# Optimization experiments

Hardware: AMD Instinct MI355X
Metric: run time of the kernel (lower is better)

Reference implementation:

```python
import jax, jax.numpy as jnp
import numpy as np

N_NODES = 100000
N_EDGES = 3200000
D_IN = 512
D_HID = 16
N_CLS = 7


def setup_inputs() -> dict:
    key = jax.random.key(0)
    k1, k2, k3, k4, k5, k6 = jax.random.split(key, 6)
    x = jax.random.normal(k1, (N_NODES, D_IN), dtype=jnp.float32)
    edge_index = jax.random.randint(k2, (2, N_EDGES), 0, N_NODES, dtype=jnp.int64)
    # Glorot-ish init for the two GCNConv layers (normalize=False)
    W1 = jax.random.normal(k3, (D_IN, D_HID), dtype=jnp.float32) / np.sqrt(D_IN)
    b1 = jnp.zeros((D_HID,), dtype=jnp.float32)
    W2 = jax.random.normal(k4, (D_HID, N_CLS), dtype=jnp.float32) / np.sqrt(D_HID)
    b2 = jnp.zeros((N_CLS,), dtype=jnp.float32)
    return {"x": x, "edge_index": edge_index, "W1": W1, "b1": b1, "W2": W2, "b2": b2}


def gcn_conv(h, src, dst, W, b, n_nodes):
    # GCNConv with normalize=False: transform, then scatter-add x_j into dst.
    h = h @ W                                   # [N, d_out]
    msg = jnp.take(h, src, axis=0)              # [E, d_out] gather from source nodes
    agg = jax.ops.segment_sum(msg, dst, num_segments=n_nodes)  # [N, d_out]
    return agg + b


def reference(x, edge_index, W1, b1, W2, b2):
    src = edge_index[0]
    dst = edge_index[1]
    h = gcn_conv(x, src, dst, W1, b1, N_NODES)
    h = jax.nn.relu(h)
    # F.dropout(training=False) in eval mode is identity; omitted (stochastic).
    out = gcn_conv(h, src, dst, W2, b2, N_NODES)
    return out
```

## Files before the change

### kernel.cpp

```cpp
#include <hip/hip_runtime.h>

#define N_NODES 100000
#define N_EDGES 3200000
#define D_IN    512
#define D_HID   16
#define N_CLS   7

__global__ __launch_bounds__(256) void zero_f4(float4* __restrict__ p, int n4) {
    int i = blockIdx.x * 256 + threadIdx.x;
    if (i < n4) p[i] = make_float4(0.f, 0.f, 0.f, 0.f);
}

__global__ __launch_bounds__(256) void gemm1(const float* __restrict__ x,
                                             const float* __restrict__ W1,
                                             float* __restrict__ h1) {
    __shared__ float4 w4s[D_IN * 4];
    const float4* W1f4 = (const float4*)W1;
    int t = threadIdx.x;
#pragma unroll
    for (int i = 0; i < 8; ++i) w4s[i * 256 + t] = W1f4[i * 256 + t];
    __syncthreads();

    int jq  = t & 3;
    int r   = t >> 2;
    int row = blockIdx.x * 64 + r;
    if (row >= N_NODES) return;

    const float4* xr = (const float4*)(x + (size_t)row * D_IN);
    float4 acc = make_float4(0.f, 0.f, 0.f, 0.f);

#pragma unroll 4
    for (int k4 = 0; k4 < D_IN / 4; ++k4) {
        float4 xv = xr[k4];
        float4 w0 = w4s[(k4 * 4 + 0) * 4 + jq];
        float4 w1 = w4s[(k4 * 4 + 1) * 4 + jq];
        float4 w2 = w4s[(k4 * 4 + 2) * 4 + jq];
        float4 w3 = w4s[(k4 * 4 + 3) * 4 + jq];
        acc.x = fmaf(xv.x, w0.x, acc.x); acc.y = fmaf(xv.x, w0.y, acc.y);
        acc.z = fmaf(xv.x, w0.z, acc.z); acc.w = fmaf(xv.x, w0.w, acc.w);
        acc.x = fmaf(xv.y, w1.x, acc.x); acc.y = fmaf(xv.y, w1.y, acc.y);
        acc.z = fmaf(xv.y, w1.z, acc.z); acc.w = fmaf(xv.y, w1.w, acc.w);
        acc.x = fmaf(xv.z, w2.x, acc.x); acc.y = fmaf(xv.z, w2.y, acc.y);
        acc.z = fmaf(xv.z, w2.z, acc.z); acc.w = fmaf(xv.z, w2.w, acc.w);
        acc.x = fmaf(xv.w, w3.x, acc.x); acc.y = fmaf(xv.w, w3.y, acc.y);
        acc.z = fmaf(xv.w, w3.z, acc.z); acc.w = fmaf(xv.w, w3.w, acc.w);
    }
    ((float4*)(h1 + (size_t)row * D_HID))[jq] = acc;
}

__global__ __launch_bounds__(256) void scatter1(const int* __restrict__ src,
                                                const int* __restrict__ dst,
                                                const float* __restrict__ h1,
                                                float* __restrict__ agg) {
    int tid = blockIdx.x * 256 + threadIdx.x;
    int e = tid >> 4;
    int j = tid & 15;
    if (e >= N_EDGES) return;
    int s = src[e];
    int d = dst[e];
    atomicAdd(&agg[(size_t)d * D_HID + j], h1[(size_t)s * D_HID + j]);
}

__global__ __launch_bounds__(256) void layer2(const float* __restrict__ agg,
                                              const float* __restrict__ b1,
                                              const float* __restrict__ W2,
                                              float* __restrict__ h2) {
    __shared__ float w2s[D_HID * N_CLS];
    __shared__ float b1s[D_HID];
    int t = threadIdx.x;
    if (t < D_HID * N_CLS) w2s[t] = W2[t];
    if (t < D_HID) b1s[t] = b1[t];
    __syncthreads();

    int n = blockIdx.x * 256 + t;
    if (n >= N_NODES) return;

    const float4* a4 = (const float4*)(agg + (size_t)n * D_HID);
    float rel[D_HID];
#pragma unroll
    for (int q = 0; q < 4; ++q) {
        float4 v = a4[q];
        rel[4 * q + 0] = fmaxf(v.x + b1s[4 * q + 0], 0.f);
        rel[4 * q + 1] = fmaxf(v.y + b1s[4 * q + 1], 0.f);
        rel[4 * q + 2] = fmaxf(v.z + b1s[4 * q + 2], 0.f);
        rel[4 * q + 3] = fmaxf(v.w + b1s[4 * q + 3], 0.f);
    }
    float o[N_CLS];
#pragma unroll
    for (int c = 0; c < N_CLS; ++c) o[c] = 0.f;
#pragma unroll
    for (int j = 0; j < D_HID; ++j) {
#pragma unroll
        for (int c = 0; c < N_CLS; ++c)
            o[c] = fmaf(rel[j], w2s[j * N_CLS + c], o[c]);
    }
    float* hp = h2 + (size_t)n * N_CLS;
#pragma unroll
    for (int c = 0; c < N_CLS; ++c) hp[c] = o[c];
}

__global__ __launch_bounds__(256) void out_init(const float* __restrict__ b2,
                                                float* __restrict__ out) {
    int i = blockIdx.x * 256 + threadIdx.x;
    if (i >= N_NODES * N_CLS) return;
    int c = i - (i / N_CLS) * N_CLS;
    out[i] = b2[c];
}

__global__ __launch_bounds__(256) void scatter2(const int* __restrict__ src,
                                                const int* __restrict__ dst,
                                                const float* __restrict__ h2,
                                                float* __restrict__ out) {
    int tid = blockIdx.x * 256 + threadIdx.x;
    if (tid >= N_EDGES * N_CLS) return;
    int e = tid / N_CLS;
    int c = tid - e * N_CLS;
    int s = src[e];
    int d = dst[e];
    atomicAdd(&out[(size_t)d * N_CLS + c], h2[(size_t)s * N_CLS + c]);
}

extern "C" void kernel_launch(void* const* d_in, const int* in_sizes, int n_in,
                              void* d_out, int out_size, void* d_ws, size_t ws_size,
                              hipStream_t stream) {
    const float* x  = (const float*)d_in[0];
    const int*   ei = (const int*)d_in[1];
    const float* W1 = (const float*)d_in[2];
    const float* b1 = (const float*)d_in[3];
    const float* W2 = (const float*)d_in[4];
    const float* b2 = (const float*)d_in[5];
    float* out = (float*)d_out;

    char* ws = (char*)d_ws;
    float* h1   = (float*)(ws);
    float* agg1 = (float*)(ws + 6400000);
    float* h2   = (float*)(ws + 12800000);

    const int* src = ei;
    const int* dst = ei + N_EDGES;

    zero_f4<<<(400000 + 255) / 256, 256, 0, stream>>>((float4*)agg1, 400000);

    gemm1<<<(N_NODES + 63) / 64, 256, 0, stream>>>(x, W1, h1);

    scatter1<<<(N_EDGES * 16) / 256, 256, 0, stream>>>(src, dst, h1, agg1);

    layer2<<<(N_NODES + 255) / 256, 256, 0, stream>>>(agg1, b1, W2, h2);

    out_init<<<(N_NODES * N_CLS + 255) / 256, 256, 0, stream>>>(b2, out);

    scatter2<<<(N_EDGES * N_CLS + 255) / 256, 256, 0, stream>>>(src, dst, h2, out);
}
```

Baseline: 713.9 us.

## Build CSR by destination and replace atomic scatters with pull-style gathers

Builds a destination-sorted CSR each call (degree histogram, single-block scan, atomic cursor fill) and replaces both per-element atomic scatter-add kernels with per-node gather kernels that accumulate in registers. The layer-2 features are padded to 8 floats so they can be written and read as aligned vectors, and the bias add is folded into the gather. This removes about 51M+22M float atomics but adds 6.4M int atomics, a serial single-block scan, and an extra pass over the edge list. Summation order per node now depends on atomic slot assignment, so results may differ slightly between runs.

New measurement: 1.049 ms. +47.0%, slower.

```diff
diff --git a/kernel.cpp b/kernel.cpp
--- a/kernel.cpp
+++ b/kernel.cpp
@@ -5,10 +5,61 @@
 #define D_IN    512
 #define D_HID   16
 #define N_CLS   7
-
-__global__ __launch_bounds__(256) void zero_f4(float4* __restrict__ p, int n4) {
+#define D_PAD   8
+
+__global__ __launch_bounds__(256) void zero_i(int* __restrict__ p, int n) {
     int i = blockIdx.x * 256 + threadIdx.x;
-    if (i < n4) p[i] = make_float4(0.f, 0.f, 0.f, 0.f);
+    if (i < n) p[i] = 0;
+}
+
+__global__ __launch_bounds__(256) void hist(const int* __restrict__ dst,
+                                            int* __restrict__ deg) {
+    int e = blockIdx.x * 256 + threadIdx.x;
+    if (e < N_EDGES) atomicAdd(&deg[dst[e]], 1);
+}
+
+__global__ __launch_bounds__(1024) void scan_offs(const int* __restrict__ deg,
+                                                  int* __restrict__ offs,
+                                                  int* __restrict__ cursor) {
+    __shared__ int part[1024];
+    const int CH = (N_NODES + 1023) / 1024;
+    int t = threadIdx.x;
+    int base = t * CH;
+    int s = 0;
+    for (int i = 0; i < CH; ++i) {
+        int idx = base + i;
+        if (idx < N_NODES) s += deg[idx];
+    }
+    part[t] = s;
+    __syncthreads();
+    for (int off = 1; off < 1024; off <<= 1) {
+        int v = 0;
+        if (t >= off) v = part[t - off];
+        __syncthreads();
+        part[t] += v;
+        __syncthreads();
+    }
+    int run = (t == 0) ? 0 : part[t - 1];
+    for (int i = 0; i < CH; ++i) {
+        int idx = base + i;
+        if (idx < N_NODES) {
+            offs[idx] = run;
+            cursor[idx] = run;
+            run += deg[idx];
+        }
+    }
+    if (t == 1023) offs[N_NODES] = part[1023];
+}
+
+__global__ __launch_bounds__(256) void fill_csr(const int* __restrict__ src,
+                                                const int* __restrict__ dst,
+                                                int* __restrict__ cursor,
+                                                int* __restrict__ esrc) {
+    int e = blockIdx.x * 256 + threadIdx.x;
+    if (e >= N_EDGES) return;
+    int d = dst[e];
+    int slot = atomicAdd(&cursor[d], 1);
+    esrc[slot] = src[e];
 }
 
 __global__ __launch_bounds__(256) void gemm1(const float* __restrict__ x,
@@ -48,23 +99,33 @@
     ((float4*)(h1 + (size_t)row * D_HID))[jq] = acc;
 }
 
-__global__ __launch_bounds__(256) void scatter1(const int* __restrict__ src,
-                                                const int* __restrict__ dst,
-                                                const float* __restrict__ h1,
-                                                float* __restrict__ agg) {
-    int tid = blockIdx.x * 256 + threadIdx.x;
-    int e = tid >> 4;
-    int j = tid & 15;
-    if (e >= N_EDGES) return;
-    int s = src[e];
-    int d = dst[e];
-    atomicAdd(&agg[(size_t)d * D_HID + j], h1[(size_t)s * D_HID + j]);
+__global__ __launch_bounds__(256) void gather1(const int* __restrict__ offs,
+                                               const int* __restrict__ esrc,
+                                               const float* __restrict__ h1,
+                                               float* __restrict__ agg) {
+    int t = threadIdx.x;
+    int j = t & 15, ln = t >> 4;
+    int node = blockIdx.x * 16 + ln;
+    if (node >= N_NODES) return;
+    int k0 = offs[node], k1 = offs[node + 1];
+    float sum = 0.f;
+    int k = k0;
+    for (; k + 1 < k1; k += 2) {
+        int s0 = esrc[k];
+        int s1 = esrc[k + 1];
+        float a = h1[s0 * D_HID + j];
+        float b = h1[s1 * D_HID + j];
+        sum += a;
+        sum += b;
+    }
+    if (k < k1) sum += h1[esrc[k] * D_HID + j];
+    agg[node * D_HID + j] = sum;
 }
 
 __global__ __launch_bounds__(256) void layer2(const float* __restrict__ agg,
                                               const float* __restrict__ b1,
                                               const float* __restrict__ W2,
-                                              float* __restrict__ h2) {
+                                              float* __restrict__ h2p) {
     __shared__ float w2s[D_HID * N_CLS];
     __shared__ float b1s[D_HID];
     int t = threadIdx.x;
@@ -85,39 +146,42 @@
         rel[4 * q + 2] = fmaxf(v.z + b1s[4 * q + 2], 0.f);
         rel[4 * q + 3] = fmaxf(v.w + b1s[4 * q + 3], 0.f);
     }
-    float o[N_CLS];
-#pragma unroll
-    for (int c = 0; c < N_CLS; ++c) o[c] = 0.f;
+    float o[D_PAD];
+#pragma unroll
+    for (int c = 0; c < D_PAD; ++c) o[c] = 0.f;
 #pragma unroll
     for (int j = 0; j < D_HID; ++j) {
 #pragma unroll
         for (int c = 0; c < N_CLS; ++c)
             o[c] = fmaf(rel[j], w2s[j * N_CLS + c], o[c]);
     }
-    float* hp = h2 + (size_t)n * N_CLS;
-#pragma unroll
-    for (int c = 0; c < N_CLS; ++c) hp[c] = o[c];
-}
-
-__global__ __launch_bounds__(256) void out_init(const float* __restrict__ b2,
-                                                float* __restrict__ out) {
-    int i = blockIdx.x * 256 + threadIdx.x;
-    if (i >= N_NODES * N_CLS) return;
-    int c = i - (i / N_CLS) * N_CLS;
-    out[i] = b2[c];
-}
-
-__global__ __launch_bounds__(256) void scatter2(const int* __restrict__ src,
-                                                const int* __restrict__ dst,
-                                                const float* __restrict__ h2,
-                                                float* __restrict__ out) {
-    int tid = blockIdx.x * 256 + threadIdx.x;
-    if (tid >= N_EDGES * N_CLS) return;
-    int e = tid / N_CLS;
-    int c = tid - e * N_CLS;
-    int s = src[e];
-    int d = dst[e];
-    atomicAdd(&out[(size_t)d * N_CLS + c], h2[(size_t)s * N_CLS + c]);
+    float4* hp = (float4*)(h2p + (size_t)n * D_PAD);
+    hp[0] = make_float4(o[0], o[1], o[2], o[3]);
+    hp[1] = make_float4(o[4], o[5], o[6], 0.f);
+}
+
+__global__ __launch_bounds__(256) void gather2(const int* __restrict__ offs,
+                                               const int* __restrict__ esrc,
+                                               const float* __restrict__ h2p,
+                                               const float* __restrict__ b2,
+                                               float* __restrict__ out) {
+    int t = threadIdx.x;
+    int j = t & 7, ln = t >> 3;
+    int node = blockIdx.x * 32 + ln;
+    if (node >= N_NODES) return;
+    int k0 = offs[node], k1 = offs[node + 1];
+    float sum = 0.f;
+    int k = k0;
+    for (; k + 1 < k1; k += 2) {
+        int s0 = esrc[k];
+        int s1 = esrc[k + 1];
+        float a = h2p[s0 * D_PAD + j];
+        float b = h2p[s1 * D_PAD + j];
+        sum += a;
+        sum += b;
+    }
+    if (k < k1) sum += h2p[esrc[k] * D_PAD + j];
+    if (j < N_CLS) out[(size_t)node * N_CLS + j] = sum + b2[j];
 }
 
 extern "C" void kernel_launch(void* const* d_in, const int* in_sizes, int n_in,
@@ -132,22 +196,27 @@
     float* out = (float*)d_out;
 
     char* ws = (char*)d_ws;
-    float* h1   = (float*)(ws);
-    float* agg1 = (float*)(ws + 6400000);
-    float* h2   = (float*)(ws + 12800000);
+    float* h1     = (float*)(ws);
+    float* agg1   = (float*)(ws + 6400000);
+    float* h2p    = (float*)(ws + 12800000);
+    int*   deg    = (int*)  (ws + 16000000);
+    int*   offs   = (int*)  (ws + 16400000);
+    int*   cursor = (int*)  (ws + 16800032);
+    int*   esrc   = (int*)  (ws + 17200032);
 
     const int* src = ei;
     const int* dst = ei + N_EDGES;
 
-    zero_f4<<<(400000 + 255) / 256, 256, 0, stream>>>((float4*)agg1, 400000);
+    zero_i   <<<(N_NODES + 255) / 256, 256, 0, stream>>>(deg, N_NODES);
+    hist     <<<(N_EDGES + 255) / 256, 256, 0, stream>>>(dst, deg);
+    scan_offs<<<1, 1024, 0, stream>>>(deg, offs, cursor);
+    fill_csr <<<(N_EDGES + 255) / 256, 256, 0, stream>>>(src, dst, cursor, esrc);
 
     gemm1<<<(N_NODES + 63) / 64, 256, 0, stream>>>(x, W1, h1);
 
-    scatter1<<<(N_EDGES * 16) / 256, 256, 0, stream>>>(src, dst, h1, agg1);
-
-    layer2<<<(N_NODES + 255) / 256, 256, 0, stream>>>(agg1, b1, W2, h2);
-
-    out_init<<<(N_NODES * N_CLS + 255) / 256, 256, 0, stream>>>(b2, out);
-
-    scatter2<<<(N_EDGES * N_CLS + 255) / 256, 256, 0, stream>>>(src, dst, h2, out);
-}
+    gather1<<<(N_NODES + 15) / 16, 256, 0, stream>>>(offs, esrc, h1, agg1);
+
+    layer2<<<(N_NODES + 255) / 256, 256, 0, stream>>>(agg1, b1, W2, h2p);
+
+    gather2<<<(N_NODES + 31) / 32, 256, 0, stream>>>(offs, esrc, h2p, b2, out);
+}
```

## Bucket edges by destination and aggregate in shared memory per node block

Applied to the files above, without the earlier changes.

Edges are first partitioned into 512 destination buckets of 196 nodes each, with source index and local node offset packed into one word. Each workgroup then aggregates its bucket with LDS atomics instead of global atomics, fusing bias, ReLU and the second linear layer, and the second aggregation writes the output with the bias added directly. Layer-2 features are padded to 8 floats for aligned gathers. The fixed bucket capacity of 8192 relies on a roughly uniform destination distribution; a skewed graph would overflow a bucket.

Measured after the change: 757.0 us. +6.0%, slower.

```diff
diff --git a/kernel.cpp b/kernel.cpp
--- a/kernel.cpp
+++ b/kernel.cpp
@@ -5,10 +5,53 @@
 #define D_IN    512
 #define D_HID   16
 #define N_CLS   7
-
-__global__ __launch_bounds__(256) void zero_f4(float4* __restrict__ p, int n4) {
-    int i = blockIdx.x * 256 + threadIdx.x;
-    if (i < n4) p[i] = make_float4(0.f, 0.f, 0.f, 0.f);
+#define D_PAD   8
+
+#define NB        512
+#define NODES_PER 196
+#define BCAP      8192
+#define FILL_CHUNK 16384
+#define FILL_WGS  ((N_EDGES + FILL_CHUNK - 1) / FILL_CHUNK)
+
+__global__ __launch_bounds__(512) void cursor_init(int* __restrict__ cursor) {
+    cursor[threadIdx.x] = (int)threadIdx.x * BCAP;
+}
+
+__global__ __launch_bounds__(1024) void bucket_fill(const int* __restrict__ src,
+                                                    const int* __restrict__ dst,
+                                                    int* __restrict__ cursor,
+                                                    unsigned int* __restrict__ packed) {
+    __shared__ int bcnt[NB];
+    __shared__ int bcur[NB];
+    int t = threadIdx.x;
+    if (t < NB) bcnt[t] = 0;
+    __syncthreads();
+
+    int base_e = blockIdx.x * FILL_CHUNK;
+#pragma unroll
+    for (int i = 0; i < FILL_CHUNK / 1024; ++i) {
+        int e = base_e + i * 1024 + t;
+        if (e < N_EDGES) atomicAdd(&bcnt[dst[e] / NODES_PER], 1);
+    }
+    __syncthreads();
+
+    if (t < NB) {
+        int c = bcnt[t];
+        bcur[t] = (c > 0) ? atomicAdd(&cursor[t], c) : 0;
+    }
+    __syncthreads();
+
+#pragma unroll
+    for (int i = 0; i < FILL_CHUNK / 1024; ++i) {
+        int e = base_e + i * 1024 + t;
+        if (e < N_EDGES) {
+            int d = dst[e];
+            int b = d / NODES_PER;
+            int loc = d - b * NODES_PER;
+            int r = atomicAdd(&bcur[b], 1);
+            packed[r] = (unsigned)src[e] | ((unsigned)loc << 17);
+        }
+    }
 }
 
 __global__ __launch_bounds__(256) void gemm1(const float* __restrict__ x,
@@ -48,76 +91,89 @@
     ((float4*)(h1 + (size_t)row * D_HID))[jq] = acc;
 }
 
-__global__ __launch_bounds__(256) void scatter1(const int* __restrict__ src,
-                                                const int* __restrict__ dst,
-                                                const float* __restrict__ h1,
-                                                float* __restrict__ agg) {
-    int tid = blockIdx.x * 256 + threadIdx.x;
-    int e = tid >> 4;
-    int j = tid & 15;
-    if (e >= N_EDGES) return;
-    int s = src[e];
-    int d = dst[e];
-    atomicAdd(&agg[(size_t)d * D_HID + j], h1[(size_t)s * D_HID + j]);
-}
-
-__global__ __launch_bounds__(256) void layer2(const float* __restrict__ agg,
-                                              const float* __restrict__ b1,
-                                              const float* __restrict__ W2,
-                                              float* __restrict__ h2) {
+__global__ __launch_bounds__(1024) void agg1_layer2(const unsigned int* __restrict__ packed,
+                                                    const int* __restrict__ cursor,
+                                                    const float* __restrict__ h1,
+                                                    const float* __restrict__ b1,
+                                                    const float* __restrict__ W2,
+                                                    float* __restrict__ h2p) {
+    __shared__ float acc[NODES_PER * D_HID];
     __shared__ float w2s[D_HID * N_CLS];
     __shared__ float b1s[D_HID];
     int t = threadIdx.x;
     if (t < D_HID * N_CLS) w2s[t] = W2[t];
-    if (t < D_HID) b1s[t] = b1[t];
-    __syncthreads();
-
-    int n = blockIdx.x * 256 + t;
-    if (n >= N_NODES) return;
-
-    const float4* a4 = (const float4*)(agg + (size_t)n * D_HID);
-    float rel[D_HID];
-#pragma unroll
-    for (int q = 0; q < 4; ++q) {
-        float4 v = a4[q];
-        rel[4 * q + 0] = fmaxf(v.x + b1s[4 * q + 0], 0.f);
-        rel[4 * q + 1] = fmaxf(v.y + b1s[4 * q + 1], 0.f);
-        rel[4 * q + 2] = fmaxf(v.z + b1s[4 * q + 2], 0.f);
-        rel[4 * q + 3] = fmaxf(v.w + b1s[4 * q + 3], 0.f);
-    }
-    float o[N_CLS];
-#pragma unroll
-    for (int c = 0; c < N_CLS; ++c) o[c] = 0.f;
-#pragma unroll
-    for (int j = 0; j < D_HID; ++j) {
-#pragma unroll
-        for (int c = 0; c < N_CLS; ++c)
-            o[c] = fmaf(rel[j], w2s[j * N_CLS + c], o[c]);
-    }
-    float* hp = h2 + (size_t)n * N_CLS;
-#pragma unroll
-    for (int c = 0; c < N_CLS; ++c) hp[c] = o[c];
-}
-
-__global__ __launch_bounds__(256) void out_init(const float* __restrict__ b2,
-                                                float* __restrict__ out) {
-    int i = blockIdx.x * 256 + threadIdx.x;
-    if (i >= N_NODES * N_CLS) return;
-    int c = i - (i / N_CLS) * N_CLS;
-    out[i] = b2[c];
-}
-
-__global__ __launch_bounds__(256) void scatter2(const int* __restrict__ src,
-                                                const int* __restrict__ dst,
-                                                const float* __restrict__ h2,
-                                                float* __restrict__ out) {
-    int tid = blockIdx.x * 256 + threadIdx.x;
-    if (tid >= N_EDGES * N_CLS) return;
-    int e = tid / N_CLS;
-    int c = tid - e * N_CLS;
-    int s = src[e];
-    int d = dst[e];
-    atomicAdd(&out[(size_t)d * N_CLS + c], h2[(size_t)s * N_CLS + c]);
+    if (t >= 128 && t < 128 + D_HID) b1s[t - 128] = b1[t - 128];
+    for (int i = t; i < NODES_PER * D_HID; i += 1024) acc[i] = 0.f;
+    __syncthreads();
+
+    int b  = blockIdx.x;
+    int e0 = b * BCAP;
+    int e1 = cursor[b];
+    int g  = t >> 4;
+    int j  = t & 15;
+    for (int k = e0 + g; k < e1; k += 64) {
+        unsigned p = packed[k];
+        int s   = p & 0x1FFFF;
+        int loc = p >> 17;
+        atomicAdd(&acc[loc * D_HID + j], h1[(size_t)s * D_HID + j]);
+    }
+    __syncthreads();
+
+    int nbase = b * NODES_PER;
+    int nn = N_NODES - nbase; if (nn > NODES_PER) nn = NODES_PER;
+    if ((int)t < nn) {
+        float o[N_CLS];
+#pragma unroll
+        for (int c = 0; c < N_CLS; ++c) o[c] = 0.f;
+#pragma unroll
+        for (int jj = 0; jj < D_HID; ++jj) {
+            float r = fmaxf(acc[t * D_HID + jj] + b1s[jj], 0.f);
+#pragma unroll
+            for (int c = 0; c < N_CLS; ++c)
+                o[c] = fmaf(r, w2s[jj * N_CLS + c], o[c]);
+        }
+        float4* hp = (float4*)(h2p + (size_t)(nbase + t) * D_PAD);
+        hp[0] = make_float4(o[0], o[1], o[2], o[3]);
+        hp[1] = make_float4(o[4], o[5], o[6], 0.f);
+    }
+}
+
+__global__ __launch_bounds__(1024) void agg2_out(const unsigned int* __restrict__ packed,
+                                                 const int* __restrict__ cursor,
+                                                 const float* __restrict__ h2p,
+                                                 const float* __restrict__ b2,
+                                                 float* __restrict__ out) {
+    __shared__ float acc[NODES_PER * D_PAD];
+    __shared__ float b2s[N_CLS];
+    int t = threadIdx.x;
+    if (t < N_CLS) b2s[t] = b2[t];
+    for (int i = t; i < NODES_PER * D_PAD; i += 1024) acc[i] = 0.f;
+    __syncthreads();
+
+    int b  = blockIdx.x;
+    int e0 = b * BCAP;
+    int e1 = cursor[b];
+    int g  = t >> 3;
+    int j  = t & 7;
+    for (int k = e0 + g; k < e1; k += 128) {
+        unsigned p = packed[k];
+        int s   = p & 0x1FFFF;
+        int loc = p >> 17;
+        atomicAdd(&acc[loc * D_PAD + j], h2p[(size_t)s * D_PAD + j]);
+    }
+    __syncthreads();
+
+    int nbase = b * NODES_PER;
+    int nn = N_NODES - nbase; if (nn > NODES_PER) nn = NODES_PER;
+    if (nn > 0) {
+        int total = nn * N_CLS;
+        float* obase = out + (size_t)nbase * N_CLS;
+        for (int i = t; i < total; i += 1024) {
+            int node = i / N_CLS;
+            int c = i - node * N_CLS;
+            obase[i] = acc[node * D_PAD + c] + b2s[c];
+        }
+    }
 }
 
 extern "C" void kernel_launch(void* const* d_in, const int* in_sizes, int n_in,
@@ -132,22 +188,17 @@
     float* out = (float*)d_out;
 
     char* ws = (char*)d_ws;
-    float* h1   = (float*)(ws);
-    float* agg1 = (float*)(ws + 6400000);
-    float* h2   = (float*)(ws + 12800000);
+    float*        h1     = (float*)(ws);
+    float*        h2p    = (float*)(ws + 6400000);
+    unsigned int* packed = (unsigned int*)(ws + 9600000);
+    int*          cursor = (int*)(ws + 26377216);
 
     const int* src = ei;
     const int* dst = ei + N_EDGES;
 
-    zero_f4<<<(400000 + 255) / 256, 256, 0, stream>>>((float4*)agg1, 400000);
-
+    cursor_init<<<1, 512, 0, stream>>>(cursor);
+    bucket_fill<<<FILL_WGS, 1024, 0, stream>>>(src, dst, cursor, packed);
     gemm1<<<(N_NODES + 63) / 64, 256, 0, stream>>>(x, W1, h1);
-
-    scatter1<<<(N_EDGES * 16) / 256, 256, 0, stream>>>(src, dst, h1, agg1);
-
-    layer2<<<(N_NODES + 255) / 256, 256, 0, stream>>>(agg1, b1, W2, h2);
-
-    out_init<<<(N_NODES * N_CLS + 255) / 256, 256, 0, stream>>>(b2, out);
-
-    scatter2<<<(N_EDGES * N_CLS + 255) / 256, 256, 0, stream>>>(src, dst, h2, out);
-}
+    agg1_layer2<<<NB, 1024, 0, stream>>>(packed, cursor, h1, b1, W2, h2p);
+    agg2_out<<<NB, 1024, 0, stream>>>(packed, cursor, h2p, b2, out);
+}
```
